# Kernel tuning notes

Measured on AMD Instinct MI355X. Metric: run time of the kernel, lower is better.

The kernel has to match this reference:

```python
import jax, jax.numpy as jnp
import numpy as np

N = 50000      # nodes
E = 800000     # edges (before self loops)
F_IN = 128     # input feature dim
H = 4          # attention heads
C = 64         # per-head channels (hidden_dim = out_channels = 64)
HC = H * C     # 256, concat output width of each GATv2Conv
G = 32         # number of graphs in the batch
NEG_SLOPE_ATT = 0.2   # GATv2 internal LeakyReLU
NEG_SLOPE_ACT = 0.01  # encoder nn.LeakyReLU() default


def _glorot(key, shape, fan_in):
    return jax.random.normal(key, shape, jnp.float32) * (1.0 / np.sqrt(fan_in))


def setup_inputs() -> dict:
    key = jax.random.key(0)
    ks = jax.random.split(key, 32)
    inp = {}
    inp["x"] = jax.random.normal(ks[0], (N, F_IN), jnp.float32)
    inp["edge_index"] = jax.random.randint(ks[1], (2, E), 0, N, jnp.int32)
    inp["batch"] = jnp.sort(jax.random.randint(ks[2], (N,), 0, G, jnp.int32))
    i = 3
    for li, fin in ((1, F_IN), (2, HC), (3, HC)):
        inp[f"Wl{li}"] = _glorot(ks[i], (HC, fin), fin); i += 1
        inp[f"bl{li}"] = jnp.zeros((HC,), jnp.float32)
        inp[f"Wr{li}"] = _glorot(ks[i], (HC, fin), fin); i += 1
        inp[f"br{li}"] = jnp.zeros((HC,), jnp.float32)
        inp[f"att{li}"] = _glorot(ks[i], (H, C), C); i += 1
        inp[f"bo{li}"] = jnp.zeros((HC,), jnp.float32)
    return inp


def _gatv2_layer(x, src, dst, Wl, bl, Wr, br, att, bo):
    n = x.shape[0]
    xl = (x @ Wl.T + bl).reshape(n, H, C)  # source transform
    xr = (x @ Wr.T + br).reshape(n, H, C)  # target transform
    # per-edge attention logits: a^T LeakyReLU(xl[j] + xr[i])
    e = jax.nn.leaky_relu(xl[src] + xr[dst], negative_slope=NEG_SLOPE_ATT)  # [E', H, C]
    score = jnp.einsum('ehc,hc->eh', e, att)                                # [E', H]
    # segment softmax over incoming edges of each destination node
    m = jax.ops.segment_max(score, dst, num_segments=n)
    p = jnp.exp(score - m[dst])
    s = jax.ops.segment_sum(p, dst, num_segments=n)
    alpha = p / s[dst]
    out = jax.ops.segment_sum(alpha[:, :, None] * xl[src], dst, num_segments=n)
    return out.reshape(n, HC) + bo


def reference(x, edge_index, batch,
              Wl1, bl1, Wr1, br1, att1, bo1,
              Wl2, bl2, Wr2, br2, att2, bo2,
              Wl3, bl3, Wr3, br3, att3, bo3):
    loop = jnp.arange(N, dtype=edge_index.dtype)
    src = jnp.concatenate([edge_index[0], loop])  # add self loops (PyG default)
    dst = jnp.concatenate([edge_index[1], loop])
    h = _gatv2_layer(x, src, dst, Wl1, bl1, Wr1, br1, att1, bo1)
    h = jax.nn.leaky_relu(h, negative_slope=NEG_SLOPE_ACT)
    h = _gatv2_layer(h, src, dst, Wl2, bl2, Wr2, br2, att2, bo2)
    h = jax.nn.leaky_relu(h, negative_slope=NEG_SLOPE_ACT)
    h = _gatv2_layer(h, src, dst, Wl3, bl3, Wr3, br3, att3, bo3)
    # global mean pool over graphs
    sums = jax.ops.segment_sum(h, batch, num_segments=G)
    cnt = jax.ops.segment_sum(jnp.ones((N,), h.dtype), batch, num_segments=G)
    return sums / jnp.maximum(cnt, 1.0)[:, None]
```

## Files before the change

kernel.cpp:

```cpp
#include <hip/hip_runtime.h>

#define HEADS 4
#define CH 64
#define HC 256
#define NGRAPH 32
#define NEG_ATT 0.2f
#define NEG_ACT 0.01f

typedef __attribute__((ext_vector_type(8))) short bf16x8;
typedef __attribute__((ext_vector_type(4))) float f32x4;
typedef __attribute__((ext_vector_type(2))) float f32x2;

typedef __attribute__((address_space(3))) unsigned int lds_u32;
typedef const __attribute__((address_space(1))) unsigned int glob_u32;

__device__ __forceinline__ void gl_lds16(const void* g, void* l) {
  __builtin_amdgcn_global_load_lds((glob_u32*)(uintptr_t)g,
                                   (lds_u32*)(unsigned int)(uintptr_t)l, 16, 0, 0);
}

__device__ __forceinline__ void split2(float a, float b, unsigned& hi, unsigned& lo) {
  unsigned ua = __float_as_uint(a), ub = __float_as_uint(b);
  float la = a - __uint_as_float(ua & 0xFFFF0000u);
  float lb = b - __uint_as_float(ub & 0xFFFF0000u);
  hi = __builtin_amdgcn_perm(ub, ua, 0x07060302u);
  lo = __builtin_amdgcn_perm(__float_as_uint(lb), __float_as_uint(la), 0x07060302u);
}

__device__ __forceinline__ unsigned rtn_bf16(float f) {
  unsigned u = __float_as_uint(f);
  return (u + 0x7FFFu + ((u >> 16) & 1u)) >> 16;
}

__global__ __launch_bounds__(256) void convert_x(
    const float* __restrict__ X, unsigned short* __restrict__ xhi,
    unsigned short* __restrict__ xlo, int total4) {
  int g = blockIdx.x * 256 + threadIdx.x;
  if (g >= total4) return;
  float4 v = *(const float4*)&X[(size_t)g * 4];
  uint2 h2, l2;
  split2(v.x, v.y, h2.x, l2.x);
  split2(v.z, v.w, h2.y, l2.y);
  *(uint2*)&xhi[(size_t)g * 4] = h2;
  *(uint2*)&xlo[(size_t)g * 4] = l2;
}

__global__ __launch_bounds__(256) void convert_w_frag(
    const float* __restrict__ Wl, const float* __restrict__ Wr,
    unsigned short* __restrict__ wfhi, unsigned short* __restrict__ wflo, int K) {
  int g = blockIdx.x * 256 + threadIdx.x;
  int lane = g & 63;
  int ct = (g >> 6) & 31;
  int kb = g >> 11;
  int col = ct * 16 + (lane & 15);
  int k = kb * 32 + (lane >> 4) * 8;
  const float* src = (col < HC) ? &Wl[(size_t)col * K + k] : &Wr[(size_t)(col - HC) * K + k];
  float4 v0 = *(const float4*)src;
  float4 v1 = *(const float4*)(src + 4);
  uint4 hq, lq;
  split2(v0.x, v0.y, hq.x, lq.x);
  split2(v0.z, v0.w, hq.y, lq.y);
  split2(v1.x, v1.y, hq.z, lq.z);
  split2(v1.z, v1.w, hq.w, lq.w);
  *(uint4*)&wfhi[(size_t)g * 8] = hq;
  *(uint4*)&wflo[(size_t)g * 8] = lq;
}

template <int K>
__global__ __launch_bounds__(256) void gemm_fused(
    const unsigned short* __restrict__ xhi, const unsigned short* __restrict__ xlo,
    const unsigned short* __restrict__ wfhi, const unsigned short* __restrict__ wflo,
    const float* __restrict__ bl, const float* __restrict__ br,
    unsigned short* __restrict__ Y1, float* __restrict__ Y2, int N) {
  constexpr int nkb = K >> 5;
  __shared__ unsigned short Ah[2][128][32];
  __shared__ unsigned short Al[2][128][32];

  const int tid = threadIdx.x;
  const int wave = tid >> 6;
  const int lane = tid & 63;
  const int quad = lane >> 4;
  const int l16 = lane & 15;
  const int wr = (wave >> 1) * 64;
  const int wc = (wave & 1) * 64;
  const int col0 = blockIdx.x * 128;
  const int row0 = blockIdx.y * 128;
  const int ctg0 = blockIdx.x * 8 + (wave & 1) * 4;

  const int c0 = tid, c1 = tid + 256;
  const int r0g = row0 + (c0 >> 2), r1g = row0 + (c1 >> 2);
  const int ko0 = (c0 & 3) * 8, ko1 = (c1 & 3) * 8;
  const int gr0 = (r0g < N) ? r0g : N - 1;
  const int gr1 = (r1g < N) ? r1g : N - 1;

  f32x4 acc[4][4];
#pragma unroll
  for (int i = 0; i < 4; i++)
#pragma unroll
    for (int j = 0; j < 4; j++) acc[i][j] = (f32x4){0.f, 0.f, 0.f, 0.f};

  bf16x8 bhi[2][4], blo[2][4];
#pragma unroll
  for (int j = 0; j < 4; j++) {
    size_t ci = (size_t)(ctg0 + j) * 64 + lane;
    bhi[0][j] = *(const bf16x8*)&wfhi[ci * 8];
    blo[0][j] = *(const bf16x8*)&wflo[ci * 8];
  }
  {
    size_t ga0 = (size_t)gr0 * K + ko0;
    size_t ga1 = (size_t)gr1 * K + ko1;
    gl_lds16(&xhi[ga0], &Ah[0][c0 >> 2][ko0]);
    gl_lds16(&xlo[ga0], &Al[0][c0 >> 2][ko0]);
    gl_lds16(&xhi[ga1], &Ah[0][c1 >> 2][ko1]);
    gl_lds16(&xlo[ga1], &Al[0][c1 >> 2][ko1]);
  }

#pragma unroll
  for (int kb = 0; kb < nkb; kb++) {
    const int cur = kb & 1, nxt = cur ^ 1;
    __syncthreads();
    if (kb + 1 < nkb) {
      int k0 = (kb + 1) * 32;
      size_t ga0 = (size_t)gr0 * K + k0 + ko0;
      size_t ga1 = (size_t)gr1 * K + k0 + ko1;
      gl_lds16(&xhi[ga0], &Ah[nxt][c0 >> 2][ko0]);
      gl_lds16(&xlo[ga0], &Al[nxt][c0 >> 2][ko0]);
      gl_lds16(&xhi[ga1], &Ah[nxt][c1 >> 2][ko1]);
      gl_lds16(&xlo[ga1], &Al[nxt][c1 >> 2][ko1]);
    }
    bf16x8 ahi[4], alo[4];
#pragma unroll
    for (int i = 0; i < 4; i++) {
      ahi[i] = *(const bf16x8*)&Ah[cur][wr + i * 16 + l16][quad * 8];
      alo[i] = *(const bf16x8*)&Al[cur][wr + i * 16 + l16][quad * 8];
    }
    if (kb + 1 < nkb) {
#pragma unroll
      for (int j = 0; j < 4; j++) {
        size_t ci = ((size_t)(kb + 1) * 32 + ctg0 + j) * 64 + lane;
        bhi[nxt][j] = *(const bf16x8*)&wfhi[ci * 8];
        blo[nxt][j] = *(const bf16x8*)&wflo[ci * 8];
      }
    }
#pragma unroll
    for (int i = 0; i < 4; i++)
#pragma unroll
      for (int j = 0; j < 4; j++) {
        acc[i][j] = __builtin_amdgcn_mfma_f32_16x16x32_bf16(ahi[i], bhi[cur][j], acc[i][j], 0, 0, 0);
        acc[i][j] = __builtin_amdgcn_mfma_f32_16x16x32_bf16(ahi[i], blo[cur][j], acc[i][j], 0, 0, 0);
        acc[i][j] = __builtin_amdgcn_mfma_f32_16x16x32_bf16(alo[i], bhi[cur][j], acc[i][j], 0, 0, 0);
      }
  }

#pragma unroll
  for (int j = 0; j < 4; j++) {
    int colg = col0 + wc + j * 16 + l16;
    if (colg < HC) {
      float bv = bl[colg];
#pragma unroll
      for (int i = 0; i < 4; i++)
#pragma unroll
        for (int r = 0; r < 4; r++) {
          int row = row0 + wr + i * 16 + quad * 4 + r;
          if (row < N)
            Y1[(size_t)row * HC + colg] = (unsigned short)rtn_bf16(acc[i][j][r] + bv);
        }
    } else {
      int cc = colg - HC;
      float bv = br[cc];
#pragma unroll
      for (int i = 0; i < 4; i++)
#pragma unroll
        for (int r = 0; r < 4; r++) {
          int row = row0 + wr + i * 16 + quad * 4 + r;
          if (row < N) Y2[(size_t)row * HC + cc] = acc[i][j][r] + bv;
        }
    }
  }
}

__global__ __launch_bounds__(256) void hist_dst(
    const int* __restrict__ edst, int* __restrict__ counts, int E) {
  int e = blockIdx.x * 256 + threadIdx.x;
  if (e < E) atomicAdd(&counts[edst[e]], 1);
}

__global__ __launch_bounds__(256) void scan_blocks(
    const int* __restrict__ counts, int* __restrict__ row_start,
    int* __restrict__ bsum, int N) {
  __shared__ int tmp[256];
  int t = threadIdx.x;
  int base = blockIdx.x * 1024 + t * 4;
  int v0 = (base     < N) ? counts[base]     + 1 : 0;
  int v1 = (base + 1 < N) ? counts[base + 1] + 1 : 0;
  int v2 = (base + 2 < N) ? counts[base + 2] + 1 : 0;
  int v3 = (base + 3 < N) ? counts[base + 3] + 1 : 0;
  int c1 = v0 + v1, c2 = c1 + v2, tot = c2 + v3;
  tmp[t] = tot;
  __syncthreads();
  for (int off = 1; off < 256; off <<= 1) {
    int add = (t >= off) ? tmp[t - off] : 0;
    __syncthreads();
    tmp[t] += add;
    __syncthreads();
  }
  int excl = tmp[t] - tot;
  if (base     < N) row_start[base + 1] = excl + v0;
  if (base + 1 < N) row_start[base + 2] = excl + c1;
  if (base + 2 < N) row_start[base + 3] = excl + c2;
  if (base + 3 < N) row_start[base + 4] = excl + tot;
  if (t == 255) bsum[blockIdx.x] = tmp[255];
  if (blockIdx.x == 0 && t == 0) row_start[0] = 0;
}

__global__ void scan_tops(int* __restrict__ bsum, int nb) {
  int lane = threadIdx.x;
  int v = (lane < nb) ? bsum[lane] : 0;
  for (int off = 1; off < 64; off <<= 1) {
    int u = __shfl_up(v, off);
    if (lane >= off) v += u;
  }
  if (lane < nb) bsum[lane] = v;
}

__global__ __launch_bounds__(256) void scan_add(
    int* __restrict__ row_start, const int* __restrict__ bsum, int N) {
  int off = bsum[blockIdx.x];
  int i = (blockIdx.x + 1) * 1024 + threadIdx.x * 4;
#pragma unroll
  for (int k = 0; k < 4; k++)
    if (i + k < N) row_start[i + k + 1] += off;
}

__global__ __launch_bounds__(256) void csr_init(
    const int* __restrict__ row_start, int* __restrict__ fill_pos,
    int* __restrict__ csr_src, int N) {
  int i = blockIdx.x * 256 + threadIdx.x;
  if (i < N) {
    int p = row_start[i];
    csr_src[p] = i << 9;
    fill_pos[i] = p + 1;
  }
}

__global__ __launch_bounds__(256) void csr_scatter(
    const int* __restrict__ esrc, const int* __restrict__ edst,
    int* __restrict__ fill_pos, int* __restrict__ csr_src, int E) {
  int e = blockIdx.x * 256 + threadIdx.x;
  if (e < E) {
    int p = atomicAdd(&fill_pos[edst[e]], 1);
    csr_src[p] = esrc[e] << 9;
  }
}

__device__ __forceinline__ void unpk(uint2 q, f32x2& v01, f32x2& v23) {
  v01.x = __uint_as_float(q.x << 16);
  v01.y = __uint_as_float(q.x & 0xFFFF0000u);
  v23.x = __uint_as_float(q.y << 16);
  v23.y = __uint_as_float(q.y & 0xFFFF0000u);
}

__device__ __forceinline__ float edot(f32x2 l01, f32x2 l23, f32x2 r01, f32x2 r23,
                                      f32x2 a01, f32x2 a23) {
  f32x2 t01 = l01 + r01, t23 = l23 + r23;
  f32x2 u01 = t01 * NEG_ATT, u23 = t23 * NEG_ATT;
  t01.x = fmaxf(t01.x, u01.x); t01.y = fmaxf(t01.y, u01.y);
  t23.x = fmaxf(t23.x, u23.x); t23.y = fmaxf(t23.y, u23.y);
  f32x2 dv = t01 * a01 + t23 * a23;
  float d = dv.x + dv.y;
  d += __shfl_xor(d, 1);
  d += __shfl_xor(d, 2);
  d += __shfl_xor(d, 4);
  d += __shfl_xor(d, 8);
  return d;
}

__global__ __launch_bounds__(256) void gat_fused(
    const unsigned short* __restrict__ xl, const float* __restrict__ xr,
    const int* __restrict__ row_start, const int* __restrict__ csr_soff,
    const float* __restrict__ att, const float* __restrict__ bo,
    float* __restrict__ outf, unsigned short* __restrict__ ohi,
    unsigned short* __restrict__ olo, int N, int split_out) {
  int dst = (blockIdx.x * 256 + threadIdx.x) >> 6;
  int lane = threadIdx.x & 63;
  if (dst >= N) return;
  int h = lane >> 4;
  int off = h * CH + (lane & 15) * 4;
  const int loff = off * 2;
  const char* xlc = (const char*)xl;
  f32x2 a01 = *(const f32x2*)&att[off];
  f32x2 a23 = *(const f32x2*)&att[off + 2];
  f32x2 r01 = *(const f32x2*)&xr[(size_t)dst * HC + off];
  f32x2 r23 = *(const f32x2*)&xr[(size_t)dst * HC + off + 2];
  f32x2 o01 = {0.f, 0.f}, o23 = {0.f, 0.f};
  float m = -__builtin_inff();
  float s = 0.f;
  int p = row_start[dst];
  int end = row_start[dst + 1];
  for (; p + 4 <= end; p += 4) {
    int b0 = csr_soff[p + 0] + loff, b1 = csr_soff[p + 1] + loff;
    int b2 = csr_soff[p + 2] + loff, b3 = csr_soff[p + 3] + loff;
    uint2 q0 = *(const uint2*)(xlc + b0);
    uint2 q1 = *(const uint2*)(xlc + b1);
    uint2 q2 = *(const uint2*)(xlc + b2);
    uint2 q3 = *(const uint2*)(xlc + b3);
    f32x2 l0a, l0b, l1a, l1b, l2a, l2b, l3a, l3b;
    unpk(q0, l0a, l0b);
    unpk(q1, l1a, l1b);
    unpk(q2, l2a, l2b);
    unpk(q3, l3a, l3b);
    float d0 = edot(l0a, l0b, r01, r23, a01, a23);
    float d1 = edot(l1a, l1b, r01, r23, a01, a23);
    float d2 = edot(l2a, l2b, r01, r23, a01, a23);
    float d3 = edot(l3a, l3b, r01, r23, a01, a23);
    float newm = fmaxf(fmaxf(fmaxf(d0, d1), fmaxf(d2, d3)), m);
    float sc = __expf(m - newm);
    float e0 = __expf(d0 - newm), e1 = __expf(d1 - newm);
    float e2 = __expf(d2 - newm), e3 = __expf(d3 - newm);
    s = fmaf(s, sc, (e0 + e1) + (e2 + e3));
    f32x2 acc01 = l0a * e0 + l1a * e1;
    acc01 = l2a * e2 + acc01;
    acc01 = l3a * e3 + acc01;
    o01 = o01 * sc + acc01;
    f32x2 acc23 = l0b * e0 + l1b * e1;
    acc23 = l2b * e2 + acc23;
    acc23 = l3b * e3 + acc23;
    o23 = o23 * sc + acc23;
    m = newm;
  }
  for (; p < end; p++) {
    int b0 = csr_soff[p] + loff;
    uint2 q0 = *(const uint2*)(xlc + b0);
    f32x2 la, lb;
    unpk(q0, la, lb);
    float d = edot(la, lb, r01, r23, a01, a23);
    float newm = fmaxf(m, d);
    float sc = __expf(m - newm);
    float pe = __expf(d - newm);
    s = fmaf(s, sc, pe);
    o01 = o01 * sc + la * pe;
    o23 = o23 * sc + lb * pe;
    m = newm;
  }
  float inv = 1.f / s;
  f32x2 b01 = *(const f32x2*)&bo[off];
  f32x2 b23 = *(const f32x2*)&bo[off + 2];
  f32x2 res01 = o01 * inv + b01;
  f32x2 res23 = o23 * inv + b23;
  if (split_out) {
    f32x2 v01 = res01 * NEG_ACT, v23 = res23 * NEG_ACT;
    res01.x = fmaxf(res01.x, v01.x); res01.y = fmaxf(res01.y, v01.y);
    res23.x = fmaxf(res23.x, v23.x); res23.y = fmaxf(res23.y, v23.y);
    uint2 h2, l2;
    split2(res01.x, res01.y, h2.x, l2.x);
    split2(res23.x, res23.y, h2.y, l2.y);
    *(uint2*)&ohi[(size_t)dst * HC + off] = h2;
    *(uint2*)&olo[(size_t)dst * HC + off] = l2;
  } else {
    float4 r4 = {res01.x, res01.y, res23.x, res23.y};
    *(float4*)&outf[(size_t)dst * HC + off] = r4;
  }
}

__global__ __launch_bounds__(256) void pool_partial(
    const float* __restrict__ h, const int* __restrict__ batch,
    float* __restrict__ out, int* __restrict__ cnt, int N) {
  __shared__ float part[NGRAPH][HC];
  __shared__ int bsh[256];
  __shared__ int cpart[NGRAPH];
  int j = threadIdx.x;
#pragma unroll
  for (int g = 0; g < NGRAPH; g++) part[g][j] = 0.f;
  if (j < NGRAPH) cpart[j] = 0;
  int n0 = blockIdx.x * 256;
  int nend = min(n0 + 256, N);
  int nj = n0 + j;
  bsh[j] = (nj < N) ? batch[nj] : 0;
  __syncthreads();
  if (nj < nend) atomicAdd(&cpart[bsh[j]], 1);
  for (int n = n0; n < nend; n++) {
    int g = bsh[n - n0];
    part[g][j] += h[(size_t)n * HC + j];
  }
  __syncthreads();
#pragma unroll
  for (int g = 0; g < NGRAPH; g++) {
    float v = part[g][j];
    if (v != 0.f) atomicAdd(&out[g * HC + j], v);
  }
  if (j < NGRAPH && cpart[j] > 0) atomicAdd(&cnt[j], cpart[j]);
}

__global__ __launch_bounds__(256) void pool_final(
    float* __restrict__ out, const int* __restrict__ cnt) {
  int g = blockIdx.x;
  int j = threadIdx.x;
  float c = (float)max(cnt[g], 1);
  out[g * HC + j] /= c;
}

extern "C" void kernel_launch(void* const* d_in, const int* in_sizes, int n_in,
                              void* d_out, int out_size, void* d_ws, size_t ws_size,
                              hipStream_t stream) {
  const float* x = (const float*)d_in[0];
  const int* ei = (const int*)d_in[1];
  const int* batch = (const int*)d_in[2];
  const int N = in_sizes[2];
  const int E = in_sizes[1] / 2;
  const int Etot = E + N;

  const float* Wl[3] = {(const float*)d_in[3], (const float*)d_in[9], (const float*)d_in[15]};
  const float* bl[3] = {(const float*)d_in[4], (const float*)d_in[10], (const float*)d_in[16]};
  const float* Wr[3] = {(const float*)d_in[5], (const float*)d_in[11], (const float*)d_in[17]};
  const float* br[3] = {(const float*)d_in[6], (const float*)d_in[12], (const float*)d_in[18]};
  const float* att[3] = {(const float*)d_in[7], (const float*)d_in[13], (const float*)d_in[19]};
  const float* bo[3] = {(const float*)d_in[8], (const float*)d_in[14], (const float*)d_in[20]};

  float* B0 = (float*)d_ws;
  float* B1 = B0 + (size_t)N * HC;
  float* B2 = B1 + (size_t)N * HC;
  unsigned short* w1hi = (unsigned short*)(B2 + (size_t)N * HC);
  unsigned short* w1lo = w1hi + 512 * 128;
  unsigned short* w2hi = w1lo + 512 * 128;
  unsigned short* w2lo = w2hi + 512 * 256;
  unsigned short* w3hi = w2lo + 512 * 256;
  unsigned short* w3lo = w3hi + 512 * 256;
  int* counts = (int*)(w3lo + 512 * 256);
  int* row_start = counts + N;
  int* bsum = row_start + N + 1;
  int* fill_pos = bsum + 64;
  int* csr_src = fill_pos + N;
  int* cnt = csr_src + Etot;

  unsigned short* xlB = (unsigned short*)B1;
  unsigned short* xhiL1 = (unsigned short*)B0;
  unsigned short* xloL1 = xhiL1 + (size_t)N * 128;
  unsigned short* xhiL = (unsigned short*)B0;
  unsigned short* xloL = xhiL + (size_t)N * HC;

  const int* esrc = ei;
  const int* edst = ei + E;

  convert_x<<<(N * 128 / 4 + 255) / 256, 256, 0, stream>>>(x, xhiL1, xloL1, N * 128 / 4);
  convert_w_frag<<<128 * 64 / 256, 256, 0, stream>>>(Wl[0], Wr[0], w1hi, w1lo, 128);
  convert_w_frag<<<256 * 64 / 256, 256, 0, stream>>>(Wl[1], Wr[1], w2hi, w2lo, 256);
  convert_w_frag<<<256 * 64 / 256, 256, 0, stream>>>(Wl[2], Wr[2], w3hi, w3lo, 256);

  const int nscan = (N + 1023) / 1024;
  (void)hipMemsetAsync(counts, 0, (size_t)N * sizeof(int), stream);
  hist_dst<<<(E + 255) / 256, 256, 0, stream>>>(edst, counts, E);
  scan_blocks<<<nscan, 256, 0, stream>>>(counts, row_start, bsum, N);
  scan_tops<<<1, 64, 0, stream>>>(bsum, nscan);
  scan_add<<<nscan - 1, 256, 0, stream>>>(row_start, bsum, N);
  csr_init<<<(N + 255) / 256, 256, 0, stream>>>(row_start, fill_pos, csr_src, N);
  csr_scatter<<<(E + 255) / 256, 256, 0, stream>>>(esrc, edst, fill_pos, csr_src, E);

  const dim3 ggrid(4, (N + 127) / 128);
  const int fblocks = (N * 64 + 255) / 256;

  gemm_fused<128><<<ggrid, 256, 0, stream>>>(xhiL1, xloL1, w1hi, w1lo, bl[0], br[0], xlB, B2, N);
  gat_fused<<<fblocks, 256, 0, stream>>>(xlB, B2, row_start, csr_src, att[0], bo[0],
                                         nullptr, xhiL, xloL, N, 1);
  gemm_fused<256><<<ggrid, 256, 0, stream>>>(xhiL, xloL, w2hi, w2lo, bl[1], br[1], xlB, B2, N);
  gat_fused<<<fblocks, 256, 0, stream>>>(xlB, B2, row_start, csr_src, att[1], bo[1],
                                         nullptr, xhiL, xloL, N, 1);
  gemm_fused<256><<<ggrid, 256, 0, stream>>>(xhiL, xloL, w3hi, w3lo, bl[2], br[2], xlB, B2, N);
  gat_fused<<<fblocks, 256, 0, stream>>>(xlB, B2, row_start, csr_src, att[2], bo[2],
                                         B0, nullptr, nullptr, N, 0);

  (void)hipMemsetAsync(d_out, 0, NGRAPH * HC * sizeof(float), stream);
  (void)hipMemsetAsync(cnt, 0, NGRAPH * sizeof(int), stream);
  pool_partial<<<(N + 255) / 256, 256, 0, stream>>>(B0, batch, (float*)d_out, cnt, N);
  pool_final<<<NGRAPH, 256, 0, stream>>>((float*)d_out, cnt);
}
```

Before: 692.1 us.

## Load GEMM A fragments directly from global and swizzle block order

The GEMM no longer stages the activation tile in LDS through global_load_lds with a block-wide barrier each k-step. Each wave now loads its A fragments straight from global memory into registers, double-buffered, so the per-k-step __syncthreads disappears. The launch grid is also flattened into a 1D grid with a swizzled mapping that groups the 4 column blocks of 8 consecutive row blocks, to improve L2 reuse of A rows. The trade-off is that both column-wave pairs now load the same A rows redundantly, which raises global/L2 traffic and register pressure.

```diff
diff --git a/kernel.cpp b/kernel.cpp
--- a/kernel.cpp
+++ b/kernel.cpp
@@ -10,14 +10,6 @@
 typedef __attribute__((ext_vector_type(8))) short bf16x8;
 typedef __attribute__((ext_vector_type(4))) float f32x4;
 typedef __attribute__((ext_vector_type(2))) float f32x2;
-
-typedef __attribute__((address_space(3))) unsigned int lds_u32;
-typedef const __attribute__((address_space(1))) unsigned int glob_u32;
-
-__device__ __forceinline__ void gl_lds16(const void* g, void* l) {
-  __builtin_amdgcn_global_load_lds((glob_u32*)(uintptr_t)g,
-                                   (lds_u32*)(unsigned int)(uintptr_t)l, 16, 0, 0);
-}
 
 __device__ __forceinline__ void split2(float a, float b, unsigned& hi, unsigned& lo) {
   unsigned ua = __float_as_uint(a), ub = __float_as_uint(b);
@@ -71,10 +63,12 @@
     const unsigned short* __restrict__ xhi, const unsigned short* __restrict__ xlo,
     const unsigned short* __restrict__ wfhi, const unsigned short* __restrict__ wflo,
     const float* __restrict__ bl, const float* __restrict__ br,
-    unsigned short* __restrict__ Y1, float* __restrict__ Y2, int N) {
+    unsigned short* __restrict__ Y1, float* __restrict__ Y2, int N, int nrb) {
   constexpr int nkb = K >> 5;
-  __shared__ unsigned short Ah[2][128][32];
-  __shared__ unsigned short Al[2][128][32];
+  const int f = blockIdx.x;
+  const int rb = (f & 7) + 8 * (f >> 5);
+  const int cb = (f >> 3) & 3;
+  if (rb >= nrb) return;
 
   const int tid = threadIdx.x;
   const int wave = tid >> 6;
@@ -83,15 +77,17 @@
   const int l16 = lane & 15;
   const int wr = (wave >> 1) * 64;
   const int wc = (wave & 1) * 64;
-  const int col0 = blockIdx.x * 128;
-  const int row0 = blockIdx.y * 128;
-  const int ctg0 = blockIdx.x * 8 + (wave & 1) * 4;
-
-  const int c0 = tid, c1 = tid + 256;
-  const int r0g = row0 + (c0 >> 2), r1g = row0 + (c1 >> 2);
-  const int ko0 = (c0 & 3) * 8, ko1 = (c1 & 3) * 8;
-  const int gr0 = (r0g < N) ? r0g : N - 1;
-  const int gr1 = (r1g < N) ? r1g : N - 1;
+  const int row0 = rb * 128;
+  const int col0 = cb * 128;
+  const int ctg0 = cb * 8 + (wave & 1) * 4;
+
+  size_t abase[4];
+#pragma unroll
+  for (int i = 0; i < 4; i++) {
+    int row = row0 + wr + i * 16 + l16;
+    if (row >= N) row = N - 1;
+    abase[i] = (size_t)row * K + quad * 8;
+  }
 
   f32x4 acc[4][4];
 #pragma unroll
@@ -99,56 +95,43 @@
 #pragma unroll
     for (int j = 0; j < 4; j++) acc[i][j] = (f32x4){0.f, 0.f, 0.f, 0.f};
 
-  bf16x8 bhi[2][4], blo[2][4];
+  bf16x8 ah[2][4], al[2][4], bh[2][4], bw[2][4];
+#pragma unroll
+  for (int i = 0; i < 4; i++) {
+    ah[0][i] = *(const bf16x8*)&xhi[abase[i]];
+    al[0][i] = *(const bf16x8*)&xlo[abase[i]];
+  }
 #pragma unroll
   for (int j = 0; j < 4; j++) {
     size_t ci = (size_t)(ctg0 + j) * 64 + lane;
-    bhi[0][j] = *(const bf16x8*)&wfhi[ci * 8];
-    blo[0][j] = *(const bf16x8*)&wflo[ci * 8];
-  }
-  {
-    size_t ga0 = (size_t)gr0 * K + ko0;
-    size_t ga1 = (size_t)gr1 * K + ko1;
-    gl_lds16(&xhi[ga0], &Ah[0][c0 >> 2][ko0]);
-    gl_lds16(&xlo[ga0], &Al[0][c0 >> 2][ko0]);
-    gl_lds16(&xhi[ga1], &Ah[0][c1 >> 2][ko1]);
-    gl_lds16(&xlo[ga1], &Al[0][c1 >> 2][ko1]);
+    bh[0][j] = *(const bf16x8*)&wfhi[ci * 8];
+    bw[0][j] = *(const bf16x8*)&wflo[ci * 8];
   }
 
 #pragma unroll
   for (int kb = 0; kb < nkb; kb++) {
     const int cur = kb & 1, nxt = cur ^ 1;
-    __syncthreads();
     if (kb + 1 < nkb) {
-      int k0 = (kb + 1) * 32;
-      size_t ga0 = (size_t)gr0 * K + k0 + ko0;
-      size_t ga1 = (size_t)gr1 * K + k0 + ko1;
-      gl_lds16(&xhi[ga0], &Ah[nxt][c0 >> 2][ko0]);
-      gl_lds16(&xlo[ga0], &Al[nxt][c0 >> 2][ko0]);
-      gl_lds16(&xhi[ga1], &Ah[nxt][c1 >> 2][ko1]);
-      gl_lds16(&xlo[ga1], &Al[nxt][c1 >> 2][ko1]);
-    }
-    bf16x8 ahi[4], alo[4];
-#pragma unroll
-    for (int i = 0; i < 4; i++) {
-      ahi[i] = *(const bf16x8*)&Ah[cur][wr + i * 16 + l16][quad * 8];
-      alo[i] = *(const bf16x8*)&Al[cur][wr + i * 16 + l16][quad * 8];
-    }
-    if (kb + 1 < nkb) {
+      const int koff = (kb + 1) * 32;
+#pragma unroll
+      for (int i = 0; i < 4; i++) {
+        ah[nxt][i] = *(const bf16x8*)&xhi[abase[i] + koff];
+        al[nxt][i] = *(const bf16x8*)&xlo[abase[i] + koff];
+      }
 #pragma unroll
       for (int j = 0; j < 4; j++) {
         size_t ci = ((size_t)(kb + 1) * 32 + ctg0 + j) * 64 + lane;
-        bhi[nxt][j] = *(const bf16x8*)&wfhi[ci * 8];
-        blo[nxt][j] = *(const bf16x8*)&wflo[ci * 8];
+        bh[nxt][j] = *(const bf16x8*)&wfhi[ci * 8];
+        bw[nxt][j] = *(const bf16x8*)&wflo[ci * 8];
       }
     }
 #pragma unroll
     for (int i = 0; i < 4; i++)
 #pragma unroll
       for (int j = 0; j < 4; j++) {
-        acc[i][j] = __builtin_amdgcn_mfma_f32_16x16x32_bf16(ahi[i], bhi[cur][j], acc[i][j], 0, 0, 0);
-        acc[i][j] = __builtin_amdgcn_mfma_f32_16x16x32_bf16(ahi[i], blo[cur][j], acc[i][j], 0, 0, 0);
-        acc[i][j] = __builtin_amdgcn_mfma_f32_16x16x32_bf16(alo[i], bhi[cur][j], acc[i][j], 0, 0, 0);
+        acc[i][j] = __builtin_amdgcn_mfma_f32_16x16x32_bf16(ah[cur][i], bh[cur][j], acc[i][j], 0, 0, 0);
+        acc[i][j] = __builtin_amdgcn_mfma_f32_16x16x32_bf16(ah[cur][i], bw[cur][j], acc[i][j], 0, 0, 0);
+        acc[i][j] = __builtin_amdgcn_mfma_f32_16x16x32_bf16(al[cur][i], bh[cur][j], acc[i][j], 0, 0, 0);
       }
   }
 
@@ -455,16 +438,17 @@
   csr_init<<<(N + 255) / 256, 256, 0, stream>>>(row_start, fill_pos, csr_src, N);
   csr_scatter<<<(E + 255) / 256, 256, 0, stream>>>(esrc, edst, fill_pos, csr_src, E);
 
-  const dim3 ggrid(4, (N + 127) / 128);
+  const int nrb = (N + 127) / 128;
+  const int gblocks = ((nrb + 7) / 8) * 32;
   const int fblocks = (N * 64 + 255) / 256;
 
-  gemm_fused<128><<<ggrid, 256, 0, stream>>>(xhiL1, xloL1, w1hi, w1lo, bl[0], br[0], xlB, B2, N);
+  gemm_fused<128><<<gblocks, 256, 0, stream>>>(xhiL1, xloL1, w1hi, w1lo, bl[0], br[0], xlB, B2, N, nrb);
   gat_fused<<<fblocks, 256, 0, stream>>>(xlB, B2, row_start, csr_src, att[0], bo[0],
                                          nullptr, xhiL, xloL, N, 1);
-  gemm_fused<256><<<ggrid, 256, 0, stream>>>(xhiL, xloL, w2hi, w2lo, bl[1], br[1], xlB, B2, N);
+  gemm_fused<256><<<gblocks, 256, 0, stream>>>(xhiL, xloL, w2hi, w2lo, bl[1], br[1], xlB, B2, N, nrb);
   gat_fused<<<fblocks, 256, 0, stream>>>(xlB, B2, row_start, csr_src, att[1], bo[1],
                                          nullptr, xhiL, xloL, N, 1);
-  gemm_fused<256><<<ggrid, 256, 0, stream>>>(xhiL, xloL, w3hi, w3lo, bl[2], br[2], xlB, B2, N);
+  gemm_fused<256><<<gblocks, 256, 0, stream>>>(xhiL, xloL, w3hi, w3lo, bl[2], br[2], xlB, B2, N, nrb);
   gat_fused<<<fblocks, 256, 0, stream>>>(xlB, B2, row_start, csr_src, att[2], bo[2],
                                          B0, nullptr, nullptr, N, 0);
 
```

After: 768.8 us. 11.1% more time.
